# Performance work log

Hardware: AMD Instinct MI355X
Metric: run time of the kernel (lower is better)

The kernel has to match this reference:

```python
import jax, jax.numpy as jnp
import numpy as np

N = 50000
E = 1_600_000
D_IN = 256
D_OUT = 256


def setup_inputs() -> dict:
    key = jax.random.key(0)
    k1, k2, k3, k4, k5 = jax.random.split(key, 5)
    x = jax.random.normal(k1, (N, D_IN), dtype=jnp.float32)
    # nn.Linear weight is [out_features, in_features], init N(0, 1/sqrt(in))
    stdv = 1.0 / np.sqrt(D_IN)
    W = jax.random.normal(k2, (D_OUT, D_IN), dtype=jnp.float32) * stdv
    edge_row = jax.random.randint(k3, (E,), 0, N, dtype=jnp.int32)
    edge_col = jax.random.randint(k4, (E,), 0, N, dtype=jnp.int32)
    # normalized adjacency values (positive, ~1/avg_degree scale)
    edge_val = jax.random.uniform(k5, (E,), dtype=jnp.float32) / 32.0
    return {"x": x, "W": W, "edge_row": edge_row, "edge_col": edge_col, "edge_val": edge_val}


def reference(x, W, edge_row, edge_col, edge_val):
    # support = input @ W.T  (nn.Linear, no bias)
    support = jnp.einsum("ni,oi->no", x, W)  # [N, D_OUT]
    # output = sparse_adj @ support : gather source rows, scale, scatter-add to dest
    msgs = support[edge_col] * edge_val[:, None]  # [E, D_OUT]
    output = jax.ops.segment_sum(msgs, edge_row, num_segments=N)  # [N, D_OUT]
    return output
```

## Files before the change

kernel.cpp:

```cpp
#include <hip/hip_runtime.h>

#define D 256
#define BIN_BLOCKS 1024
#define GEMM_ROWS 64
#define LDB 40
#define MAXDEG 96

typedef float f32x4  __attribute__((ext_vector_type(4)));
typedef short bf16x8 __attribute__((ext_vector_type(8)));

__device__ __forceinline__ unsigned short f2bf(float f) {
    unsigned u = __float_as_uint(f);
    u += 0x7fffu + ((u >> 16) & 1u);
    return (unsigned short)(u >> 16);
}
__device__ __forceinline__ float bf2f(unsigned short h) {
    return __uint_as_float(((unsigned)h) << 16);
}

__global__ __launch_bounds__(256) void fused_bin_gemm(
        const float* __restrict__ x, const float* __restrict__ W,
        unsigned short* __restrict__ suppb, int n_rows,
        const int* __restrict__ erow, const int* __restrict__ ecol,
        const float* __restrict__ eval, int* __restrict__ cnt,
        unsigned* __restrict__ bins, int E) {
    __shared__ short As[GEMM_ROWS * LDB];
    __shared__ short Ws[D * LDB];

    if (blockIdx.x < BIN_BLOCKS) {
        const int stride = BIN_BLOCKS * 256;
        int e = blockIdx.x * 256 + threadIdx.x;
        for (; e + 3 * stride < E; e += 4 * stride) {
            const int d0 = erow[e];
            const int d1 = erow[e + stride];
            const int d2 = erow[e + 2 * stride];
            const int d3 = erow[e + 3 * stride];
            const unsigned b0 = ((unsigned)f2bf(eval[e])              << 16) | (unsigned)ecol[e];
            const unsigned b1 = ((unsigned)f2bf(eval[e + stride])     << 16) | (unsigned)ecol[e + stride];
            const unsigned b2 = ((unsigned)f2bf(eval[e + 2 * stride]) << 16) | (unsigned)ecol[e + 2 * stride];
            const unsigned b3 = ((unsigned)f2bf(eval[e + 3 * stride]) << 16) | (unsigned)ecol[e + 3 * stride];
            const int r0 = atomicAdd(&cnt[d0], 1);
            const int r1 = atomicAdd(&cnt[d1], 1);
            const int r2 = atomicAdd(&cnt[d2], 1);
            const int r3 = atomicAdd(&cnt[d3], 1);
            if (r0 < MAXDEG) bins[d0 * MAXDEG + r0] = b0;
            if (r1 < MAXDEG) bins[d1 * MAXDEG + r1] = b1;
            if (r2 < MAXDEG) bins[d2 * MAXDEG + r2] = b2;
            if (r3 < MAXDEG) bins[d3 * MAXDEG + r3] = b3;
        }
        for (; e < E; e += stride) {
            const int dst = erow[e];
            const int r = atomicAdd(&cnt[dst], 1);
            if (r < MAXDEG)
                bins[dst * MAXDEG + r] =
                    ((unsigned)f2bf(eval[e]) << 16) | (unsigned)ecol[e];
        }
        return;
    }

    const int m0   = (blockIdx.x - BIN_BLOCKS) * GEMM_ROWS;
    const int t    = threadIdx.x;
    const int lane = t & 63;
    const int w    = t >> 6;
    const int fr   = lane & 15;
    const int oct  = lane >> 4;

    f32x4 acc[16];
#pragma unroll
    for (int nt = 0; nt < 16; ++nt) acc[nt] = (f32x4){0.f, 0.f, 0.f, 0.f};

    const int ar = t >> 2;
    const int ac = (t & 3) * 8;

    for (int k0 = 0; k0 < D; k0 += 32) {
        {
            const int gm = m0 + ar;
            float4 a0 = {0.f, 0.f, 0.f, 0.f}, a1 = {0.f, 0.f, 0.f, 0.f};
            if (gm < n_rows) {
                a0 = *(const float4*)(x + (size_t)gm * D + k0 + ac);
                a1 = *(const float4*)(x + (size_t)gm * D + k0 + ac + 4);
            }
            ushort4 u0, u1;
            u0.x = f2bf(a0.x); u0.y = f2bf(a0.y); u0.z = f2bf(a0.z); u0.w = f2bf(a0.w);
            u1.x = f2bf(a1.x); u1.y = f2bf(a1.y); u1.z = f2bf(a1.z); u1.w = f2bf(a1.w);
            *(ushort4*)(&As[ar * LDB + ac])     = u0;
            *(ushort4*)(&As[ar * LDB + ac + 4]) = u1;
        }
        {
            const float* src = W + (size_t)t * D + k0;
#pragma unroll
            for (int q = 0; q < 4; ++q) {
                const float4 a = *(const float4*)(src + q * 8);
                const float4 b = *(const float4*)(src + q * 8 + 4);
                ushort4 u, v;
                u.x = f2bf(a.x); u.y = f2bf(a.y); u.z = f2bf(a.z); u.w = f2bf(a.w);
                v.x = f2bf(b.x); v.y = f2bf(b.y); v.z = f2bf(b.z); v.w = f2bf(b.w);
                *(ushort4*)(&Ws[t * LDB + q * 8])     = u;
                *(ushort4*)(&Ws[t * LDB + q * 8 + 4]) = v;
            }
        }
        __syncthreads();

        const bf16x8 afrag = *(const bf16x8*)(&As[(w * 16 + fr) * LDB + oct * 8]);
#pragma unroll
        for (int nt = 0; nt < 16; ++nt) {
            const bf16x8 bfrag = *(const bf16x8*)(&Ws[(nt * 16 + fr) * LDB + oct * 8]);
            acc[nt] = __builtin_amdgcn_mfma_f32_16x16x32_bf16(afrag, bfrag, acc[nt], 0, 0, 0);
        }
        __syncthreads();
    }

#pragma unroll
    for (int nt = 0; nt < 16; ++nt) {
#pragma unroll
        for (int r = 0; r < 4; ++r) {
            const int gm = m0 + w * 16 + oct * 4 + r;
            if (gm < n_rows)
                suppb[(size_t)gm * D + nt * 16 + fr] = f2bf(acc[nt][r]);
        }
    }
}

__global__ __launch_bounds__(256) void spmm_pull(const int* __restrict__ cnt,
                                                 const unsigned int* __restrict__ bins,
                                                 const unsigned short* __restrict__ supp,
                                                 float* __restrict__ out, int n) {
    const int lane4 = (threadIdx.x & 63) * 4;
    const int row   = blockIdx.x * 4 + (threadIdx.x >> 6);
    if (row >= n) return;

    int i = row * MAXDEG;
    const int deg = min(cnt[row], MAXDEG);
    const int e = i + deg;
    float ax = 0.f, ay = 0.f, az = 0.f, aw = 0.f;

    for (; i + 7 < e; i += 8) {
        unsigned p[8];
        ushort4  s[8];
#pragma unroll
        for (int j = 0; j < 8; ++j) p[j] = __builtin_nontemporal_load(&bins[i + j]);
#pragma unroll
        for (int j = 0; j < 8; ++j)
            s[j] = *(const ushort4*)(supp + (size_t)(p[j] & 0xFFFFu) * D + lane4);
#pragma unroll
        for (int j = 0; j < 8; ++j) {
            const float v = bf2f((unsigned short)(p[j] >> 16));
            ax = fmaf(bf2f(s[j].x), v, ax); ay = fmaf(bf2f(s[j].y), v, ay);
            az = fmaf(bf2f(s[j].z), v, az); aw = fmaf(bf2f(s[j].w), v, aw);
        }
    }
    for (; i < e; ++i) {
        const unsigned p0 = __builtin_nontemporal_load(&bins[i]);
        const ushort4 s0 = *(const ushort4*)(supp + (size_t)(p0 & 0xFFFFu) * D + lane4);
        const float v0 = bf2f((unsigned short)(p0 >> 16));
        ax = fmaf(bf2f(s0.x), v0, ax); ay = fmaf(bf2f(s0.y), v0, ay);
        az = fmaf(bf2f(s0.z), v0, az); aw = fmaf(bf2f(s0.w), v0, aw);
    }
    float* o = out + (size_t)row * D + lane4;
    __builtin_nontemporal_store(ax, o + 0);
    __builtin_nontemporal_store(ay, o + 1);
    __builtin_nontemporal_store(az, o + 2);
    __builtin_nontemporal_store(aw, o + 3);
}

__global__ __launch_bounds__(256) void spmm_scatter(const int* __restrict__ erow,
                                                    const int* __restrict__ ecol,
                                                    const float* __restrict__ eval,
                                                    const unsigned short* __restrict__ supp,
                                                    float* __restrict__ out, int E) {
    const int lane4 = (threadIdx.x & 63) * 4;
    const int wid  = (int)((blockIdx.x * blockDim.x + threadIdx.x) >> 6);
    const int nw   = (int)((gridDim.x * blockDim.x) >> 6);
    for (int e = wid; e < E; e += nw) {
        const int   dst = erow[e];
        const int   src = ecol[e];
        const float v   = eval[e];
        const ushort4 s = *(const ushort4*)(supp + (size_t)src * D + lane4);
        float* o = out + (size_t)dst * D + lane4;
        atomicAdd(o + 0, bf2f(s.x) * v);
        atomicAdd(o + 1, bf2f(s.y) * v);
        atomicAdd(o + 2, bf2f(s.z) * v);
        atomicAdd(o + 3, bf2f(s.w) * v);
    }
}

extern "C" void kernel_launch(void* const* d_in, const int* in_sizes, int n_in,
                              void* d_out, int out_size, void* d_ws, size_t ws_size,
                              hipStream_t stream) {
    const float* x    = (const float*)d_in[0];
    const float* W    = (const float*)d_in[1];
    const int*   erow = (const int*)d_in[2];
    const int*   ecol = (const int*)d_in[3];
    const float* eval = (const float*)d_in[4];
    float*       out  = (float*)d_out;

    const int n = in_sizes[0] / D;
    const int E = in_sizes[2];
    const int nbm = (n + GEMM_ROWS - 1) / GEMM_ROWS;

    size_t off = 0;
    auto take = [&](size_t bytes) {
        char* p = (char*)d_ws + off;
        off += (bytes + 255) & ~(size_t)255;
        return (void*)p;
    };
    unsigned short* suppb = (unsigned short*)take((size_t)n * D * 2);
    int*      cnt  = (int*)take((size_t)n * sizeof(int));
    unsigned* bins = (unsigned*)take((size_t)n * MAXDEG * sizeof(unsigned));
    const bool slots_ok = (off <= ws_size);

    if (slots_ok) {
        hipMemsetAsync(cnt, 0, (size_t)n * sizeof(int), stream);
        fused_bin_gemm<<<BIN_BLOCKS + nbm, 256, 0, stream>>>(
            x, W, suppb, n, erow, ecol, eval, cnt, bins, E);
        spmm_pull<<<(n + 3) / 4, 256, 0, stream>>>(cnt, bins, suppb, out, n);
    } else {
        hipMemsetAsync(d_out, 0, (size_t)out_size * sizeof(float), stream);
        fused_bin_gemm<<<BIN_BLOCKS + nbm, 256, 0, stream>>>(
            x, W, suppb, n, erow, ecol, eval, (int*)d_ws, nullptr, 0);
        spmm_scatter<<<4096, 256, 0, stream>>>(erow, ecol, eval, suppb, out, E);
    }
}
```

Baseline: 277.5 us.

## Split edge binning into atomic rank pass and separate scatter kernel

The fused binning blocks now only do the per-destination atomic counter increments and record each edge's rank. A new edge_bin kernel then reads erow, ecol, eval and rank and writes the packed (bf16 value, column) entries into the fixed-width bins. The aim is to make the atomic phase lighter so it overlaps better with the GEMM blocks. The cost is an extra kernel launch, an extra E-sized rank buffer that is written and then read back, and erow being read twice.

```diff
diff --git a/kernel.cpp b/kernel.cpp
--- a/kernel.cpp
+++ b/kernel.cpp
@@ -1,7 +1,7 @@
 #include <hip/hip_runtime.h>
 
 #define D 256
-#define BIN_BLOCKS 1024
+#define HIST_BLOCKS 1024
 #define GEMM_ROWS 64
 #define LDB 40
 #define MAXDEG 96
@@ -18,47 +18,37 @@
     return __uint_as_float(((unsigned)h) << 16);
 }
 
-__global__ __launch_bounds__(256) void fused_bin_gemm(
+__global__ __launch_bounds__(256) void hist_gemm(
         const float* __restrict__ x, const float* __restrict__ W,
         unsigned short* __restrict__ suppb, int n_rows,
-        const int* __restrict__ erow, const int* __restrict__ ecol,
-        const float* __restrict__ eval, int* __restrict__ cnt,
-        unsigned* __restrict__ bins, int E) {
+        const int* __restrict__ erow, int* __restrict__ cnt,
+        int* __restrict__ rank, int E) {
     __shared__ short As[GEMM_ROWS * LDB];
     __shared__ short Ws[D * LDB];
 
-    if (blockIdx.x < BIN_BLOCKS) {
-        const int stride = BIN_BLOCKS * 256;
+    if (blockIdx.x < HIST_BLOCKS) {
+        const int stride = HIST_BLOCKS * 256;
         int e = blockIdx.x * 256 + threadIdx.x;
         for (; e + 3 * stride < E; e += 4 * stride) {
             const int d0 = erow[e];
             const int d1 = erow[e + stride];
             const int d2 = erow[e + 2 * stride];
             const int d3 = erow[e + 3 * stride];
-            const unsigned b0 = ((unsigned)f2bf(eval[e])              << 16) | (unsigned)ecol[e];
-            const unsigned b1 = ((unsigned)f2bf(eval[e + stride])     << 16) | (unsigned)ecol[e + stride];
-            const unsigned b2 = ((unsigned)f2bf(eval[e + 2 * stride]) << 16) | (unsigned)ecol[e + 2 * stride];
-            const unsigned b3 = ((unsigned)f2bf(eval[e + 3 * stride]) << 16) | (unsigned)ecol[e + 3 * stride];
             const int r0 = atomicAdd(&cnt[d0], 1);
             const int r1 = atomicAdd(&cnt[d1], 1);
             const int r2 = atomicAdd(&cnt[d2], 1);
             const int r3 = atomicAdd(&cnt[d3], 1);
-            if (r0 < MAXDEG) bins[d0 * MAXDEG + r0] = b0;
-            if (r1 < MAXDEG) bins[d1 * MAXDEG + r1] = b1;
-            if (r2 < MAXDEG) bins[d2 * MAXDEG + r2] = b2;
-            if (r3 < MAXDEG) bins[d3 * MAXDEG + r3] = b3;
-        }
-        for (; e < E; e += stride) {
-            const int dst = erow[e];
-            const int r = atomicAdd(&cnt[dst], 1);
-            if (r < MAXDEG)
-                bins[dst * MAXDEG + r] =
-                    ((unsigned)f2bf(eval[e]) << 16) | (unsigned)ecol[e];
-        }
+            rank[e]              = r0;
+            rank[e + stride]     = r1;
+            rank[e + 2 * stride] = r2;
+            rank[e + 3 * stride] = r3;
+        }
+        for (; e < E; e += stride)
+            rank[e] = atomicAdd(&cnt[erow[e]], 1);
         return;
     }
 
-    const int m0   = (blockIdx.x - BIN_BLOCKS) * GEMM_ROWS;
+    const int m0   = (blockIdx.x - HIST_BLOCKS) * GEMM_ROWS;
     const int t    = threadIdx.x;
     const int lane = t & 63;
     const int w    = t >> 6;
@@ -121,6 +111,20 @@
     }
 }
 
+__global__ __launch_bounds__(256) void edge_bin(
+        const int* __restrict__ erow, const int* __restrict__ ecol,
+        const float* __restrict__ eval, const int* __restrict__ rank,
+        unsigned* __restrict__ bins, int E) {
+    int e = blockIdx.x * 256 + threadIdx.x;
+    const int stride = gridDim.x * 256;
+    for (; e < E; e += stride) {
+        const int r = rank[e];
+        if (r < MAXDEG)
+            bins[erow[e] * MAXDEG + r] =
+                ((unsigned)f2bf(eval[e]) << 16) | (unsigned)ecol[e];
+    }
+}
+
 __global__ __launch_bounds__(256) void spmm_pull(const int* __restrict__ cnt,
                                                  const unsigned int* __restrict__ bins,
                                                  const unsigned short* __restrict__ supp,
@@ -130,8 +134,7 @@
     if (row >= n) return;
 
     int i = row * MAXDEG;
-    const int deg = min(cnt[row], MAXDEG);
-    const int e = i + deg;
+    const int e = i + min(cnt[row], MAXDEG);
     float ax = 0.f, ay = 0.f, az = 0.f, aw = 0.f;
 
     for (; i + 7 < e; i += 8) {
@@ -206,18 +209,20 @@
     };
     unsigned short* suppb = (unsigned short*)take((size_t)n * D * 2);
     int*      cnt  = (int*)take((size_t)n * sizeof(int));
+    int*      rank = (int*)take((size_t)E * sizeof(int));
     unsigned* bins = (unsigned*)take((size_t)n * MAXDEG * sizeof(unsigned));
     const bool slots_ok = (off <= ws_size);
 
     if (slots_ok) {
         hipMemsetAsync(cnt, 0, (size_t)n * sizeof(int), stream);
-        fused_bin_gemm<<<BIN_BLOCKS + nbm, 256, 0, stream>>>(
-            x, W, suppb, n, erow, ecol, eval, cnt, bins, E);
+        hist_gemm<<<HIST_BLOCKS + nbm, 256, 0, stream>>>(
+            x, W, suppb, n, erow, cnt, rank, E);
+        edge_bin<<<2048, 256, 0, stream>>>(erow, ecol, eval, rank, bins, E);
         spmm_pull<<<(n + 3) / 4, 256, 0, stream>>>(cnt, bins, suppb, out, n);
     } else {
         hipMemsetAsync(d_out, 0, (size_t)out_size * sizeof(float), stream);
-        fused_bin_gemm<<<BIN_BLOCKS + nbm, 256, 0, stream>>>(
-            x, W, suppb, n, erow, ecol, eval, (int*)d_ws, nullptr, 0);
+        hist_gemm<<<HIST_BLOCKS + nbm, 256, 0, stream>>>(
+            x, W, suppb, n, erow, (int*)d_ws, (int*)d_ws, 0);
         spmm_scatter<<<4096, 256, 0, stream>>>(erow, ecol, eval, suppb, out, E);
     }
 }
```

New measurement: 250.9 us. 1.11x faster.

## Pad bin counters, chunk edges per wave, widen GEMM blocks to 512 threads

Applied to the files above, without the earlier changes.

Pads each per-node degree counter to its own 64-byte slot so that atomics on different nodes no longer share cache lines. The edge binning now gives each wave a contiguous chunk of edges and writes bins with nontemporal stores. The fused kernel moves to 512-thread blocks with 128-row GEMM tiles, and the W tile load is remapped to two threads per W row. The cost is a counter array sixteen times larger, which also enlarges the memset and makes each spmm_pull count read fetch mostly padding.

```diff
diff --git a/kernel.cpp b/kernel.cpp
--- a/kernel.cpp
+++ b/kernel.cpp
@@ -1,10 +1,11 @@
 #include <hip/hip_runtime.h>
 
 #define D 256
-#define BIN_BLOCKS 1024
-#define GEMM_ROWS 64
+#define HB_BLOCKS 256
+#define GEMM_ROWS 128
 #define LDB 40
 #define MAXDEG 96
+#define CPAD 16
 
 typedef float f32x4  __attribute__((ext_vector_type(4)));
 typedef short bf16x8 __attribute__((ext_vector_type(8)));
@@ -18,7 +19,7 @@
     return __uint_as_float(((unsigned)h) << 16);
 }
 
-__global__ __launch_bounds__(256) void fused_bin_gemm(
+__global__ __launch_bounds__(512) void histbin_gemm(
         const float* __restrict__ x, const float* __restrict__ W,
         unsigned short* __restrict__ suppb, int n_rows,
         const int* __restrict__ erow, const int* __restrict__ ecol,
@@ -27,38 +28,46 @@
     __shared__ short As[GEMM_ROWS * LDB];
     __shared__ short Ws[D * LDB];
 
-    if (blockIdx.x < BIN_BLOCKS) {
-        const int stride = BIN_BLOCKS * 256;
-        int e = blockIdx.x * 256 + threadIdx.x;
-        for (; e + 3 * stride < E; e += 4 * stride) {
-            const int d0 = erow[e];
-            const int d1 = erow[e + stride];
-            const int d2 = erow[e + 2 * stride];
-            const int d3 = erow[e + 3 * stride];
-            const unsigned b0 = ((unsigned)f2bf(eval[e])              << 16) | (unsigned)ecol[e];
-            const unsigned b1 = ((unsigned)f2bf(eval[e + stride])     << 16) | (unsigned)ecol[e + stride];
-            const unsigned b2 = ((unsigned)f2bf(eval[e + 2 * stride]) << 16) | (unsigned)ecol[e + 2 * stride];
-            const unsigned b3 = ((unsigned)f2bf(eval[e + 3 * stride]) << 16) | (unsigned)ecol[e + 3 * stride];
-            const int r0 = atomicAdd(&cnt[d0], 1);
-            const int r1 = atomicAdd(&cnt[d1], 1);
-            const int r2 = atomicAdd(&cnt[d2], 1);
-            const int r3 = atomicAdd(&cnt[d3], 1);
-            if (r0 < MAXDEG) bins[d0 * MAXDEG + r0] = b0;
-            if (r1 < MAXDEG) bins[d1 * MAXDEG + r1] = b1;
-            if (r2 < MAXDEG) bins[d2 * MAXDEG + r2] = b2;
-            if (r3 < MAXDEG) bins[d3 * MAXDEG + r3] = b3;
-        }
-        for (; e < E; e += stride) {
+    if (blockIdx.x < HB_BLOCKS) {
+        const int wid  = (blockIdx.x * 512 + threadIdx.x) >> 6;
+        const int lane = threadIdx.x & 63;
+        const int nw   = HB_BLOCKS * 8;
+        const int chunk = (E + nw - 1) / nw;
+        const int s    = wid * chunk;
+        const int end  = min(s + chunk, E);
+
+        int e = s + lane;
+        for (; e + 192 < end; e += 256) {
+            int dst[4], col[4]; float val[4];
+#pragma unroll
+            for (int j = 0; j < 4; ++j) {
+                dst[j] = erow[e + j * 64];
+                col[j] = ecol[e + j * 64];
+                val[j] = eval[e + j * 64];
+            }
+            int r[4];
+#pragma unroll
+            for (int j = 0; j < 4; ++j)
+                r[j] = atomicAdd(&cnt[dst[j] * CPAD], 1);
+#pragma unroll
+            for (int j = 0; j < 4; ++j)
+                if (r[j] < MAXDEG)
+                    __builtin_nontemporal_store(
+                        ((unsigned)f2bf(val[j]) << 16) | (unsigned)col[j],
+                        &bins[dst[j] * MAXDEG + r[j]]);
+        }
+        for (; e < end; e += 64) {
             const int dst = erow[e];
-            const int r = atomicAdd(&cnt[dst], 1);
+            const int r = atomicAdd(&cnt[dst * CPAD], 1);
             if (r < MAXDEG)
-                bins[dst * MAXDEG + r] =
-                    ((unsigned)f2bf(eval[e]) << 16) | (unsigned)ecol[e];
+                __builtin_nontemporal_store(
+                    ((unsigned)f2bf(eval[e]) << 16) | (unsigned)ecol[e],
+                    &bins[dst * MAXDEG + r]);
         }
         return;
     }
 
-    const int m0   = (blockIdx.x - BIN_BLOCKS) * GEMM_ROWS;
+    const int m0   = (blockIdx.x - HB_BLOCKS) * GEMM_ROWS;
     const int t    = threadIdx.x;
     const int lane = t & 63;
     const int w    = t >> 6;
@@ -71,6 +80,8 @@
 
     const int ar = t >> 2;
     const int ac = (t & 3) * 8;
+    const int wc = t >> 1;
+    const int wk = (t & 1) * 16;
 
     for (int k0 = 0; k0 < D; k0 += 32) {
         {
@@ -87,17 +98,20 @@
             *(ushort4*)(&As[ar * LDB + ac + 4]) = u1;
         }
         {
-            const float* src = W + (size_t)t * D + k0;
-#pragma unroll
-            for (int q = 0; q < 4; ++q) {
-                const float4 a = *(const float4*)(src + q * 8);
-                const float4 b = *(const float4*)(src + q * 8 + 4);
-                ushort4 u, v;
-                u.x = f2bf(a.x); u.y = f2bf(a.y); u.z = f2bf(a.z); u.w = f2bf(a.w);
-                v.x = f2bf(b.x); v.y = f2bf(b.y); v.z = f2bf(b.z); v.w = f2bf(b.w);
-                *(ushort4*)(&Ws[t * LDB + q * 8])     = u;
-                *(ushort4*)(&Ws[t * LDB + q * 8 + 4]) = v;
-            }
+            const float* src = W + (size_t)wc * D + k0 + wk;
+            const float4 f0 = ((const float4*)src)[0];
+            const float4 f1 = ((const float4*)src)[1];
+            const float4 f2 = ((const float4*)src)[2];
+            const float4 f3 = ((const float4*)src)[3];
+            ushort4 u0, u1, u2, u3;
+            u0.x = f2bf(f0.x); u0.y = f2bf(f0.y); u0.z = f2bf(f0.z); u0.w = f2bf(f0.w);
+            u1.x = f2bf(f1.x); u1.y = f2bf(f1.y); u1.z = f2bf(f1.z); u1.w = f2bf(f1.w);
+            u2.x = f2bf(f2.x); u2.y = f2bf(f2.y); u2.z = f2bf(f2.z); u2.w = f2bf(f2.w);
+            u3.x = f2bf(f3.x); u3.y = f2bf(f3.y); u3.z = f2bf(f3.z); u3.w = f2bf(f3.w);
+            *(ushort4*)(&Ws[wc * LDB + wk])      = u0;
+            *(ushort4*)(&Ws[wc * LDB + wk + 4])  = u1;
+            *(ushort4*)(&Ws[wc * LDB + wk + 8])  = u2;
+            *(ushort4*)(&Ws[wc * LDB + wk + 12]) = u3;
         }
         __syncthreads();
 
@@ -130,8 +144,7 @@
     if (row >= n) return;
 
     int i = row * MAXDEG;
-    const int deg = min(cnt[row], MAXDEG);
-    const int e = i + deg;
+    const int e = i + min(cnt[row * CPAD], MAXDEG);
     float ax = 0.f, ay = 0.f, az = 0.f, aw = 0.f;
 
     for (; i + 7 < e; i += 8) {
@@ -205,18 +218,18 @@
         return (void*)p;
     };
     unsigned short* suppb = (unsigned short*)take((size_t)n * D * 2);
-    int*      cnt  = (int*)take((size_t)n * sizeof(int));
+    int*      cnt  = (int*)take((size_t)n * CPAD * sizeof(int));
     unsigned* bins = (unsigned*)take((size_t)n * MAXDEG * sizeof(unsigned));
     const bool slots_ok = (off <= ws_size);
 
     if (slots_ok) {
-        hipMemsetAsync(cnt, 0, (size_t)n * sizeof(int), stream);
-        fused_bin_gemm<<<BIN_BLOCKS + nbm, 256, 0, stream>>>(
+        hipMemsetAsync(cnt, 0, (size_t)n * CPAD * sizeof(int), stream);
+        histbin_gemm<<<HB_BLOCKS + nbm, 512, 0, stream>>>(
             x, W, suppb, n, erow, ecol, eval, cnt, bins, E);
         spmm_pull<<<(n + 3) / 4, 256, 0, stream>>>(cnt, bins, suppb, out, n);
     } else {
         hipMemsetAsync(d_out, 0, (size_t)out_size * sizeof(float), stream);
-        fused_bin_gemm<<<BIN_BLOCKS + nbm, 256, 0, stream>>>(
+        histbin_gemm<<<HB_BLOCKS + nbm, 512, 0, stream>>>(
             x, W, suppb, n, erow, ecol, eval, (int*)d_ws, nullptr, 0);
         spmm_scatter<<<4096, 256, 0, stream>>>(erow, ecol, eval, suppb, out, E);
     }
```

Result: faster. 255.0 us (-8.1%).
